# Kernel optimization log

Measured on AMD Instinct MI355X. Metric: run time of the kernel, lower is better.

The kernel has to match this reference:

```python
import jax, jax.numpy as jnp
import numpy as np

IN_F = 4096
OUT_F = 11008
GROUP = 128
BATCH = 32
Q_OUT = OUT_F // 2          # two int4 values packed per byte along out dim
N_GROUPS = IN_F // GROUP    # 32 groups


def setup_inputs() -> dict:
    key = jax.random.key(0)
    k1, k2, k3, k4, k5 = jax.random.split(key, 5)
    inp = jax.random.normal(k1, (BATCH, 1, IN_F), dtype=jnp.float32)
    qweight = jax.random.randint(k2, (IN_F, Q_OUT), 0, 256, dtype=jnp.int32)   # packed bytes
    scales = jax.random.uniform(k3, (N_GROUPS, OUT_F), dtype=jnp.float32) * 0.01
    qzeros = jax.random.randint(k4, (N_GROUPS, Q_OUT), 0, 256, dtype=jnp.int32)  # packed bytes
    bias = jax.random.normal(k5, (OUT_F,), dtype=jnp.float32)
    return {"input": inp, "qweight": qweight, "scales": scales, "qzeros": qzeros, "bias": bias}


def _unpack_int4(packed, n_out):
    # packed: [rows, n_out//2] bytes; low nibble -> even out col, high nibble -> odd out col
    low = packed & 0xF
    high = (packed >> 4) & 0xF
    return jnp.stack([low, high], axis=-1).reshape(packed.shape[0], n_out)


def reference(input, qweight, scales, qzeros, bias):
    # GPTQ-style grouped dequant: w[k, n] = (q[k, n] - zero[g(k), n]) * scale[g(k), n]
    q = _unpack_int4(qweight, OUT_F).astype(jnp.float32)   # [K, N]
    z = _unpack_int4(qzeros, OUT_F).astype(jnp.float32)    # [G, N]
    gidx = jnp.arange(IN_F) // GROUP                       # [K] group index per input channel
    w = (q - z[gidx]) * scales[gidx]                       # [K, N] dequantized weight
    # decode GEMV/GEMM: [B, 1, K] x [K, N] -> [B, 1, N], plus bias (mm_bias_int4 path)
    return jnp.einsum('bsk,kn->bsn', input, w) + bias
```

## Files before the change

kernel.cpp:

```cpp
#include <hip/hip_runtime.h>
#include <cstdint>

#define IN_F 4096
#define OUT_F 11008
#define Q_OUT 5504
#define GROUP 128
#define BATCH 32

#define BN 128
#define BK 64
#define BROW 68

typedef __bf16 bf16x8 __attribute__((ext_vector_type(8)));
typedef float  f32x4  __attribute__((ext_vector_type(4)));

__global__ __launch_bounds__(256)
void xprep_kernel(const float* __restrict__ x, bf16x8* __restrict__ xf)
{
    const int t    = blockIdx.x * 256 + threadIdx.x;
    const int lane = t & 63;
    const int f    = (t >> 6) & 1;
    const int S    = t >> 7;
    const int m    = f * 16 + (lane & 15);
    const int k0   = S * 32 + (lane >> 4) * 8;
    const float4* xr = reinterpret_cast<const float4*>(x + (size_t)m * IN_F + k0);
    float4 a = xr[0], b = xr[1];
    bf16x8 v;
    v[0] = (__bf16)a.x; v[1] = (__bf16)a.y; v[2] = (__bf16)a.z; v[3] = (__bf16)a.w;
    v[4] = (__bf16)b.x; v[5] = (__bf16)b.y; v[6] = (__bf16)b.z; v[7] = (__bf16)b.w;
    xf[t] = v;
}

template<int GPB>
__global__ __launch_bounds__(256)
void int4_gemm_kernel(const uint4* __restrict__ xf,
                      const int*   __restrict__ qw,
                      const float* __restrict__ scales,
                      const int*   __restrict__ qz,
                      float*       __restrict__ partial)
{
    constexpr int NCH = GPB * 2;
    const int tid  = threadIdx.x;
    const int lane = tid & 63;
    const int wid  = tid >> 6;
    const int nb   = blockIdx.x;
    const int kb   = blockIdx.y;
    const int g0   = kb * GPB;
    const int k0b  = g0 * GROUP;

    __shared__ uint4 a_lds[2][256];
    __shared__ int   b_lds[2][64 * BROW];

    const int cl = lane & 15;
    const int kg = lane >> 4;
    const int sh = (cl & 1) * 4;

    float scv[2][GPB], zsv[2][GPB];
    #pragma unroll
    for (int nf = 0; nf < 2; ++nf) {
        const int n = nb * BN + wid * 32 + nf * 16 + cl;
        #pragma unroll
        for (int g = 0; g < GPB; ++g) {
            const float s = scales[(size_t)(g0 + g) * OUT_F + n];
            const int   z = (qz[(size_t)(g0 + g) * Q_OUT + (n >> 1)] >> sh) & 15;
            scv[nf][g] = s;
            zsv[nf][g] = s * (float)z;
        }
    }

    uint4 areg;
    int4  breg[4];
    const int bw4 = (tid & 15) * 4;
    const int bkl = tid >> 4;

    f32x4 acc[2][2] = {};

    auto LOADG = [&](int c) {
        areg = xf[(size_t)(k0b / 32 + c * 2) * 128 + tid];
        const int krow = k0b + c * BK + bkl;
        #pragma unroll
        for (int r = 0; r < 4; ++r)
            breg[r] = *reinterpret_cast<const int4*>(
                qw + (size_t)(krow + 16 * r) * Q_OUT + nb * 64 + bw4);
    };
    auto WLDS = [&](int buf) {
        a_lds[buf][tid] = areg;
        #pragma unroll
        for (int r = 0; r < 4; ++r) {
            const int k = bkl + 16 * r;
            b_lds[buf][(bw4 + 0) * BROW + k] = breg[r].x;
            b_lds[buf][(bw4 + 1) * BROW + k] = breg[r].y;
            b_lds[buf][(bw4 + 2) * BROW + k] = breg[r].z;
            b_lds[buf][(bw4 + 3) * BROW + k] = breg[r].w;
        }
    };

    LOADG(0);
    WLDS(0);
    __syncthreads();

    #pragma unroll
    for (int c = 0; c < NCH; ++c) {
        const int cur = c & 1;
        if (c + 1 < NCH) LOADG(c + 1);

        const int gl = c >> 1;
        #pragma unroll
        for (int s = 0; s < 2; ++s) {
            bf16x8 af0 = __builtin_bit_cast(bf16x8, a_lds[cur][(s * 2 + 0) * 64 + lane]);
            bf16x8 af1 = __builtin_bit_cast(bf16x8, a_lds[cur][(s * 2 + 1) * 64 + lane]);
            #pragma unroll
            for (int nf = 0; nf < 2; ++nf) {
                const int wloc = wid * 16 + nf * 8 + (cl >> 1);
                const int base = wloc * BROW + s * 32 + kg * 8;
                int4 q0 = *reinterpret_cast<const int4*>(&b_lds[cur][base]);
                int4 q1 = *reinterpret_cast<const int4*>(&b_lds[cur][base + 4]);
                const float ss = scv[nf][gl], zz = zsv[nf][gl];
                bf16x8 bfr;
                bfr[0] = (__bf16)fmaf((float)((q0.x >> sh) & 15), ss, -zz);
                bfr[1] = (__bf16)fmaf((float)((q0.y >> sh) & 15), ss, -zz);
                bfr[2] = (__bf16)fmaf((float)((q0.z >> sh) & 15), ss, -zz);
                bfr[3] = (__bf16)fmaf((float)((q0.w >> sh) & 15), ss, -zz);
                bfr[4] = (__bf16)fmaf((float)((q1.x >> sh) & 15), ss, -zz);
                bfr[5] = (__bf16)fmaf((float)((q1.y >> sh) & 15), ss, -zz);
                bfr[6] = (__bf16)fmaf((float)((q1.z >> sh) & 15), ss, -zz);
                bfr[7] = (__bf16)fmaf((float)((q1.w >> sh) & 15), ss, -zz);
                acc[0][nf] = __builtin_amdgcn_mfma_f32_16x16x32_bf16(af0, bfr, acc[0][nf], 0, 0, 0);
                acc[1][nf] = __builtin_amdgcn_mfma_f32_16x16x32_bf16(af1, bfr, acc[1][nf], 0, 0, 0);
            }
        }
        if (c + 1 < NCH) WLDS(cur ^ 1);
        __syncthreads();
    }

    #pragma unroll
    for (int f = 0; f < 2; ++f)
        #pragma unroll
        for (int nf = 0; nf < 2; ++nf) {
            const int n = nb * BN + wid * 32 + nf * 16 + cl;
            const int m = f * 16 + kg * 4;
            float* pp = partial + ((size_t)(kb * BATCH + m)) * OUT_F + n;
            pp[0]                 = acc[f][nf][0];
            pp[(size_t)OUT_F]     = acc[f][nf][1];
            pp[(size_t)OUT_F * 2] = acc[f][nf][2];
            pp[(size_t)OUT_F * 3] = acc[f][nf][3];
        }
}

__global__ __launch_bounds__(256)
void reduce_bias_kernel(const float* __restrict__ partial,
                        const float* __restrict__ bias,
                        float* __restrict__ out, int kbn)
{
    const int i4 = (blockIdx.x * 256 + threadIdx.x) * 4;
    const int n  = i4 % OUT_F;
    float4 s = *reinterpret_cast<const float4*>(bias + n);
    for (int kb = 0; kb < kbn; ++kb) {
        float4 p = *reinterpret_cast<const float4*>(partial + (size_t)kb * BATCH * OUT_F + i4);
        s.x += p.x; s.y += p.y; s.z += p.z; s.w += p.w;
    }
    *reinterpret_cast<float4*>(out + i4) = s;
}

extern "C" void kernel_launch(void* const* d_in, const int* in_sizes, int n_in,
                              void* d_out, int out_size, void* d_ws, size_t ws_size,
                              hipStream_t stream)
{
    const float* inp    = (const float*)d_in[0];
    const int*   qw     = (const int*)d_in[1];
    const float* scales = (const float*)d_in[2];
    const int*   qz     = (const int*)d_in[3];
    const float* bias   = (const float*)d_in[4];
    float*       out    = (float*)d_out;

    const size_t XFB = (size_t)BATCH * IN_F * 2;
    const size_t P_PER_KB = (size_t)BATCH * OUT_F * 4;

    bf16x8* xf      = (bf16x8*)d_ws;
    float*  partial = (float*)((char*)d_ws + XFB);

    int KBv;
    if      (ws_size >= XFB + 8 * P_PER_KB) KBv = 8;
    else if (ws_size >= XFB + 4 * P_PER_KB) KBv = 4;
    else                                    KBv = 2;

    xprep_kernel<<<64, 256, 0, stream>>>(inp, xf);

    if (KBv == 8)
        int4_gemm_kernel<4><<<dim3(OUT_F / BN, 8), 256, 0, stream>>>(
            (const uint4*)xf, qw, scales, qz, partial);
    else if (KBv == 4)
        int4_gemm_kernel<8><<<dim3(OUT_F / BN, 4), 256, 0, stream>>>(
            (const uint4*)xf, qw, scales, qz, partial);
    else
        int4_gemm_kernel<16><<<dim3(OUT_F / BN, 2), 256, 0, stream>>>(
            (const uint4*)xf, qw, scales, qz, partial);

    reduce_bias_kernel<<<(BATCH * OUT_F) / 1024, 256, 0, stream>>>(partial, bias, out, KBv);
}
```

Baseline: 34.88 us.

## Switch to fp16 MFMA with magic-number int4 dequant and narrower N tiles

Result: faster. 31.21 us (-10.5%).

```diff
diff --git a/kernel.cpp b/kernel.cpp
--- a/kernel.cpp
+++ b/kernel.cpp
@@ -1,4 +1,5 @@
 #include <hip/hip_runtime.h>
+#include <hip/hip_fp16.h>
 #include <cstdint>
 
 #define IN_F 4096
@@ -7,15 +8,17 @@
 #define GROUP 128
 #define BATCH 32
 
-#define BN 128
-#define BK 64
-#define BROW 68
+#define KBS 8
+#define GPB 4
+#define NCH 8
+#define BN 64
+#define BROWS 66
 
-typedef __bf16 bf16x8 __attribute__((ext_vector_type(8)));
-typedef float  f32x4  __attribute__((ext_vector_type(4)));
+typedef _Float16 f16x8 __attribute__((ext_vector_type(8)));
+typedef float    f32x4 __attribute__((ext_vector_type(4)));
 
 __global__ __launch_bounds__(256)
-void xprep_kernel(const float* __restrict__ x, bf16x8* __restrict__ xf)
+void xprep_kernel(const float* __restrict__ x, uint4* __restrict__ xf)
 {
     const int t    = blockIdx.x * 256 + threadIdx.x;
     const int lane = t & 63;
@@ -25,13 +28,14 @@
     const int k0   = S * 32 + (lane >> 4) * 8;
     const float4* xr = reinterpret_cast<const float4*>(x + (size_t)m * IN_F + k0);
     float4 a = xr[0], b = xr[1];
-    bf16x8 v;
-    v[0] = (__bf16)a.x; v[1] = (__bf16)a.y; v[2] = (__bf16)a.z; v[3] = (__bf16)a.w;
-    v[4] = (__bf16)b.x; v[5] = (__bf16)b.y; v[6] = (__bf16)b.z; v[7] = (__bf16)b.w;
-    xf[t] = v;
+    union { _Float16 h[8]; uint4 u; } v;
+    v.h[0] = (_Float16)a.x; v.h[1] = (_Float16)a.y;
+    v.h[2] = (_Float16)a.z; v.h[3] = (_Float16)a.w;
+    v.h[4] = (_Float16)b.x; v.h[5] = (_Float16)b.y;
+    v.h[6] = (_Float16)b.z; v.h[7] = (_Float16)b.w;
+    xf[t] = v.u;
 }
 
-template<int GPB>
 __global__ __launch_bounds__(256)
 void int4_gemm_kernel(const uint4* __restrict__ xf,
                       const int*   __restrict__ qw,
@@ -39,7 +43,6 @@
                       const int*   __restrict__ qz,
                       float*       __restrict__ partial)
 {
-    constexpr int NCH = GPB * 2;
     const int tid  = threadIdx.x;
     const int lane = tid & 63;
     const int wid  = tid >> 6;
@@ -48,114 +51,118 @@
     const int g0   = kb * GPB;
     const int k0b  = g0 * GROUP;
 
-    __shared__ uint4 a_lds[2][256];
-    __shared__ int   b_lds[2][64 * BROW];
+    __shared__ int b_lds[2][32 * BROWS];
 
-    const int cl = lane & 15;
-    const int kg = lane >> 4;
-    const int sh = (cl & 1) * 4;
+    const int cl  = lane & 15;
+    const int kg  = lane >> 4;
+    const int w   = wid * 8 + (cl >> 1);
+    const int shn = (cl & 1) * 4;
 
-    float scv[2][GPB], zsv[2][GPB];
+    const int n = nb * BN + wid * 16 + cl;
+    uint    zmu[GPB];
+    __half2 spk[GPB];
     #pragma unroll
-    for (int nf = 0; nf < 2; ++nf) {
-        const int n = nb * BN + wid * 32 + nf * 16 + cl;
-        #pragma unroll
-        for (int g = 0; g < GPB; ++g) {
-            const float s = scales[(size_t)(g0 + g) * OUT_F + n];
-            const int   z = (qz[(size_t)(g0 + g) * Q_OUT + (n >> 1)] >> sh) & 15;
-            scv[nf][g] = s;
-            zsv[nf][g] = s * (float)z;
-        }
+    for (int g = 0; g < GPB; ++g) {
+        const float s = scales[(size_t)(g0 + g) * OUT_F + n];
+        const int   z = (qz[(size_t)(g0 + g) * Q_OUT + (n >> 1)] >> shn) & 15;
+        spk[g] = __float2half2_rn(s);
+        zmu[g] = 0x64006400u + (uint)z * 0x00010001u;
     }
 
-    uint4 areg;
-    int4  breg[4];
-    const int bw4 = (tid & 15) * 4;
-    const int bkl = tid >> 4;
+    const int a8 = tid & 7;
+    const int bk = tid >> 3;
 
-    f32x4 acc[2][2] = {};
+    f32x4 acc[2] = {};
+    uint4 A[2][4];
+    uint4 b0r, b1r;
 
-    auto LOADG = [&](int c) {
-        areg = xf[(size_t)(k0b / 32 + c * 2) * 128 + tid];
-        const int krow = k0b + c * BK + bkl;
-        #pragma unroll
-        for (int r = 0; r < 4; ++r)
-            breg[r] = *reinterpret_cast<const int4*>(
-                qw + (size_t)(krow + 16 * r) * Q_OUT + nb * 64 + bw4);
+    auto LOADA = [&](int c, int buf) {
+        const size_t base = (size_t)(k0b / 32 + c * 2) * 128;
+        A[buf][0] = xf[base +   0 + lane];
+        A[buf][1] = xf[base +  64 + lane];
+        A[buf][2] = xf[base + 128 + lane];
+        A[buf][3] = xf[base + 192 + lane];
+    };
+    auto LOADB = [&](int c) {
+        const int kr = k0b + c * 64;
+        b0r = *reinterpret_cast<const uint4*>(qw + (size_t)(kr + bk)      * Q_OUT + nb * 32 + a8 * 4);
+        b1r = *reinterpret_cast<const uint4*>(qw + (size_t)(kr + bk + 32) * Q_OUT + nb * 32 + a8 * 4);
     };
     auto WLDS = [&](int buf) {
-        a_lds[buf][tid] = areg;
-        #pragma unroll
-        for (int r = 0; r < 4; ++r) {
-            const int k = bkl + 16 * r;
-            b_lds[buf][(bw4 + 0) * BROW + k] = breg[r].x;
-            b_lds[buf][(bw4 + 1) * BROW + k] = breg[r].y;
-            b_lds[buf][(bw4 + 2) * BROW + k] = breg[r].z;
-            b_lds[buf][(bw4 + 3) * BROW + k] = breg[r].w;
-        }
+        int* p = b_lds[buf];
+        p[(4 * a8 + 0) * BROWS + bk] = b0r.x;
+        p[(4 * a8 + 1) * BROWS + bk] = b0r.y;
+        p[(4 * a8 + 2) * BROWS + bk] = b0r.z;
+        p[(4 * a8 + 3) * BROWS + bk] = b0r.w;
+        p[(4 * a8 + 0) * BROWS + bk + 32] = b1r.x;
+        p[(4 * a8 + 1) * BROWS + bk + 32] = b1r.y;
+        p[(4 * a8 + 2) * BROWS + bk + 32] = b1r.z;
+        p[(4 * a8 + 3) * BROWS + bk + 32] = b1r.w;
     };
 
-    LOADG(0);
+    LOADA(0, 0);
+    LOADB(0);
     WLDS(0);
     __syncthreads();
 
     #pragma unroll
     for (int c = 0; c < NCH; ++c) {
         const int cur = c & 1;
-        if (c + 1 < NCH) LOADG(c + 1);
+        if (c + 1 < NCH) { LOADA(c + 1, cur ^ 1); LOADB(c + 1); }
 
-        const int gl = c >> 1;
+        const int     gl  = c >> 1;
+        const __half2 zmh = __builtin_bit_cast(__half2, zmu[gl]);
+        const __half2 sg  = spk[gl];
+
         #pragma unroll
         for (int s = 0; s < 2; ++s) {
-            bf16x8 af0 = __builtin_bit_cast(bf16x8, a_lds[cur][(s * 2 + 0) * 64 + lane]);
-            bf16x8 af1 = __builtin_bit_cast(bf16x8, a_lds[cur][(s * 2 + 1) * 64 + lane]);
+            const int* bp = &b_lds[cur][w * BROWS + s * 32 + kg * 8];
+            int2 q0 = *reinterpret_cast<const int2*>(bp + 0);
+            int2 q1 = *reinterpret_cast<const int2*>(bp + 2);
+            int2 q2 = *reinterpret_cast<const int2*>(bp + 4);
+            int2 q3 = *reinterpret_cast<const int2*>(bp + 6);
+
+            union { uint u[4]; f16x8 v; } bf;
+            const int2 qq[4] = {q0, q1, q2, q3};
             #pragma unroll
-            for (int nf = 0; nf < 2; ++nf) {
-                const int wloc = wid * 16 + nf * 8 + (cl >> 1);
-                const int base = wloc * BROW + s * 32 + kg * 8;
-                int4 q0 = *reinterpret_cast<const int4*>(&b_lds[cur][base]);
-                int4 q1 = *reinterpret_cast<const int4*>(&b_lds[cur][base + 4]);
-                const float ss = scv[nf][gl], zz = zsv[nf][gl];
-                bf16x8 bfr;
-                bfr[0] = (__bf16)fmaf((float)((q0.x >> sh) & 15), ss, -zz);
-                bfr[1] = (__bf16)fmaf((float)((q0.y >> sh) & 15), ss, -zz);
-                bfr[2] = (__bf16)fmaf((float)((q0.z >> sh) & 15), ss, -zz);
-                bfr[3] = (__bf16)fmaf((float)((q0.w >> sh) & 15), ss, -zz);
-                bfr[4] = (__bf16)fmaf((float)((q1.x >> sh) & 15), ss, -zz);
-                bfr[5] = (__bf16)fmaf((float)((q1.y >> sh) & 15), ss, -zz);
-                bfr[6] = (__bf16)fmaf((float)((q1.z >> sh) & 15), ss, -zz);
-                bfr[7] = (__bf16)fmaf((float)((q1.w >> sh) & 15), ss, -zz);
-                acc[0][nf] = __builtin_amdgcn_mfma_f32_16x16x32_bf16(af0, bfr, acc[0][nf], 0, 0, 0);
-                acc[1][nf] = __builtin_amdgcn_mfma_f32_16x16x32_bf16(af1, bfr, acc[1][nf], 0, 0, 0);
+            for (int t = 0; t < 4; ++t) {
+                uint pr = __builtin_amdgcn_perm((uint)qq[t].y, (uint)qq[t].x, 0x0C040C00u);
+                pr >>= shn;
+                uint qk = (pr & 0x000F000Fu) | 0x64006400u;
+                __half2 wv = __hmul2(__hsub2(__builtin_bit_cast(__half2, qk), zmh), sg);
+                bf.u[t] = __builtin_bit_cast(uint, wv);
             }
+            f16x8 af0 = __builtin_bit_cast(f16x8, A[cur][s * 2 + 0]);
+            f16x8 af1 = __builtin_bit_cast(f16x8, A[cur][s * 2 + 1]);
+            acc[0] = __builtin_amdgcn_mfma_f32_16x16x32_f16(af0, bf.v, acc[0], 0, 0, 0);
+            acc[1] = __builtin_amdgcn_mfma_f32_16x16x32_f16(af1, bf.v, acc[1], 0, 0, 0);
         }
+
         if (c + 1 < NCH) WLDS(cur ^ 1);
         __syncthreads();
     }
 
     #pragma unroll
-    for (int f = 0; f < 2; ++f)
-        #pragma unroll
-        for (int nf = 0; nf < 2; ++nf) {
-            const int n = nb * BN + wid * 32 + nf * 16 + cl;
-            const int m = f * 16 + kg * 4;
-            float* pp = partial + ((size_t)(kb * BATCH + m)) * OUT_F + n;
-            pp[0]                 = acc[f][nf][0];
-            pp[(size_t)OUT_F]     = acc[f][nf][1];
-            pp[(size_t)OUT_F * 2] = acc[f][nf][2];
-            pp[(size_t)OUT_F * 3] = acc[f][nf][3];
-        }
+    for (int f = 0; f < 2; ++f) {
+        const int m = f * 16 + kg * 4;
+        float* pp = partial + ((size_t)(kb * BATCH + m)) * OUT_F + n;
+        pp[0]                 = acc[f][0];
+        pp[(size_t)OUT_F]     = acc[f][1];
+        pp[(size_t)OUT_F * 2] = acc[f][2];
+        pp[(size_t)OUT_F * 3] = acc[f][3];
+    }
 }
 
 __global__ __launch_bounds__(256)
 void reduce_bias_kernel(const float* __restrict__ partial,
                         const float* __restrict__ bias,
-                        float* __restrict__ out, int kbn)
+                        float* __restrict__ out)
 {
     const int i4 = (blockIdx.x * 256 + threadIdx.x) * 4;
     const int n  = i4 % OUT_F;
     float4 s = *reinterpret_cast<const float4*>(bias + n);
-    for (int kb = 0; kb < kbn; ++kb) {
+    #pragma unroll
+    for (int kb = 0; kb < KBS; ++kb) {
         float4 p = *reinterpret_cast<const float4*>(partial + (size_t)kb * BATCH * OUT_F + i4);
         s.x += p.x; s.y += p.y; s.z += p.z; s.w += p.w;
     }
@@ -174,27 +181,13 @@
     float*       out    = (float*)d_out;
 
     const size_t XFB = (size_t)BATCH * IN_F * 2;
-    const size_t P_PER_KB = (size_t)BATCH * OUT_F * 4;
-
-    bf16x8* xf      = (bf16x8*)d_ws;
-    float*  partial = (float*)((char*)d_ws + XFB);
-
-    int KBv;
-    if      (ws_size >= XFB + 8 * P_PER_KB) KBv = 8;
-    else if (ws_size >= XFB + 4 * P_PER_KB) KBv = 4;
-    else                                    KBv = 2;
+    uint4* xf      = (uint4*)d_ws;
+    float* partial = (float*)((char*)d_ws + XFB);
 
     xprep_kernel<<<64, 256, 0, stream>>>(inp, xf);
 
-    if (KBv == 8)
-        int4_gemm_kernel<4><<<dim3(OUT_F / BN, 8), 256, 0, stream>>>(
-            (const uint4*)xf, qw, scales, qz, partial);
-    else if (KBv == 4)
-        int4_gemm_kernel<8><<<dim3(OUT_F / BN, 4), 256, 0, stream>>>(
-            (const uint4*)xf, qw, scales, qz, partial);
-    else
-        int4_gemm_kernel<16><<<dim3(OUT_F / BN, 2), 256, 0, stream>>>(
-            (const uint4*)xf, qw, scales, qz, partial);
+    int4_gemm_kernel<<<dim3(OUT_F / BN, KBS), 256, 0, stream>>>(
+        xf, qw, scales, qz, partial);
 
-    reduce_bias_kernel<<<(BATCH * OUT_F) / 1024, 256, 0, stream>>>(partial, bias, out, KBv);
+    reduce_bias_kernel<<<(BATCH * OUT_F) / 1024, 256, 0, stream>>>(partial, bias, out);
 }
```
